# Optimization experiments

Measured on AMD Instinct MI355X. Metric: run time of the kernel, lower is better.

## Reference

```python
import jax, jax.numpy as jnp
import numpy as np

MODES = 256


def setup_inputs() -> dict:
    key = jax.random.key(0)
    k1, k2, k3, k4, k5 = jax.random.split(key, 5)
    B, C_IN, C_OUT, N, KM = 8, 128, 128, 8192, 32
    scale = 1.0 / (C_IN * C_OUT)
    return {
        "x": jax.random.normal(k1, (B, C_IN, N), dtype=jnp.float32),
        "wbases": jax.random.normal(k2, (B, N, MODES), dtype=jnp.float32),
        "bases": jax.random.normal(k3, (B, N, MODES), dtype=jnp.float32),
        "weights": scale * jax.random.normal(k4, (C_IN, C_OUT, KM), dtype=jnp.float32),
        "D": jax.random.normal(k5, (KM, MODES), dtype=jnp.float32),
    }


def reference(x, wbases, bases, weights, D):
    # Project onto weighted bases: (b, c_in, n) x (b, n, modes) -> (b, c_in, modes)
    x_hat = jnp.einsum('bcx,bxk->bck', x, wbases[:, :, :MODES])
    # D-weighted channel mixing. Original: x_hat1[b,i,j,k] = x_hat[b,i,k]*D[j,k];
    # y[b,o,k] = sum_{i,j} x_hat1[b,i,j,k] * weights[i,o,j]
    # Equivalent fused contraction (same math, no 4D broadcast):
    y_hat = jnp.einsum('bik,jk,ioj->bok', x_hat, D, weights)
    # Reconstruct on output bases: (b, c_out, modes) x (b, n, modes) -> (b, c_out, n)
    y = jnp.einsum('bck,bxk->bcx', y_hat, bases[:, :, :MODES])
    return y
```

## Files before the change

### kernel.cpp

```cpp
#include <hip/hip_runtime.h>

#define B_    8
#define CIN   128
#define COUT  128
#define NX    8192
#define KMJ   32
#define MODES 256

typedef short bf16x8 __attribute__((ext_vector_type(8)));
typedef float f32x4  __attribute__((ext_vector_type(4)));

__device__ __forceinline__ float bf2f(unsigned short u) {
    union { unsigned int i; float f; } v; v.i = ((unsigned int)u) << 16; return v.f;
}
__device__ __forceinline__ unsigned short f2bf(float f) {
    union { float f; unsigned int i; } v; v.f = f;
    unsigned int x = v.i;
    return (unsigned short)((x + 0x7fffu + ((x >> 16) & 1u)) >> 16);
}
__device__ __forceinline__ bf16x8 cvt8(const float* __restrict__ p) {
    f32x4 a = *(const f32x4*)p;
    f32x4 b = *(const f32x4*)(p + 4);
    bf16x8 r;
    r[0] = (short)f2bf(a[0]); r[1] = (short)f2bf(a[1]);
    r[2] = (short)f2bf(a[2]); r[3] = (short)f2bf(a[3]);
    r[4] = (short)f2bf(b[0]); r[5] = (short)f2bf(b[1]);
    r[6] = (short)f2bf(b[2]); r[7] = (short)f2bf(b[3]);
    return r;
}
__device__ __forceinline__ ushort4 cvt4(f32x4 a) {
    ushort4 r;
    r.x = f2bf(a[0]); r.y = f2bf(a[1]); r.z = f2bf(a[2]); r.w = f2bf(a[3]);
    return r;
}

__global__ __launch_bounds__(256) void k1_wk(const float* __restrict__ W,
                                             const float* __restrict__ D,
                                             unsigned short* __restrict__ Wk) {
    int wave = threadIdx.x >> 6, lane = threadIdx.x & 63;
    int quad = lane >> 4, l16 = lane & 15;
    int gw  = blockIdx.x * 4 + wave;
    int oi0 = gw * 16;
    int i0  = oi0 & 127, o0 = oi0 >> 7;
    bf16x8 bfrag = cvt8(W + ((size_t)(i0 + l16) * COUT + o0) * KMJ + quad * 8);
    for (int mt = 0; mt < 16; mt++) {
        int k0 = mt * 16;
        bf16x8 afrag;
#pragma unroll
        for (int jj = 0; jj < 8; jj++)
            afrag[jj] = (short)f2bf(D[(quad * 8 + jj) * MODES + k0 + l16]);
        f32x4 acc = {0.f, 0.f, 0.f, 0.f};
        acc = __builtin_amdgcn_mfma_f32_16x16x32_bf16(afrag, bfrag, acc, 0, 0, 0);
#pragma unroll
        for (int r = 0; r < 4; r++)
            Wk[(size_t)(k0 + quad * 4 + r) * (CIN * COUT) + oi0 + l16] = f2bf(acc[r]);
    }
}

__global__ __launch_bounds__(512, 4) void k2_xhat(const float* __restrict__ X,
                                                  const float* __restrict__ WB,
                                                  unsigned short* __restrict__ PART) {
    __shared__ __align__(16) unsigned short Xs[128 * 72];
    __shared__ __align__(16) unsigned short WBT[128 * 72];
    int nt = blockIdx.x, b = blockIdx.y, kh = blockIdx.z;
    int r0 = nt * 256;
    int t  = threadIdx.x;
    int wave = t >> 6, lane = t & 63;
    int wm = wave >> 2, wk = wave & 3;
    int quad = lane >> 4, l16 = lane & 15;

    const float* xb  = X  + (size_t)b * CIN * NX;
    const float* wbb = WB + (size_t)b * NX * MODES + kh * 128;

    bool isX = (t >= 256);
    int j  = t & 255;
    int xc = j & 127, xh = j >> 7;
    int kq = j & 31,  ng = j >> 5;

    f32x4 acc[4][2];
#pragma unroll
    for (int i = 0; i < 4; i++)
#pragma unroll
        for (int jj = 0; jj < 2; jj++) acc[i][jj] = (f32x4){0.f, 0.f, 0.f, 0.f};

    f32x4 st[8];

    {
        int rs = r0;
        if (isX) {
#pragma unroll
            for (int q = 0; q < 8; q++)
                st[q] = *(const f32x4*)(xb + (size_t)xc * NX + rs + xh * 32 + 4 * q);
        } else {
#pragma unroll
            for (int g = 0; g < 2; g++)
#pragma unroll
                for (int r = 0; r < 4; r++)
                    st[g * 4 + r] = *(const f32x4*)(wbb + (size_t)(rs + g * 32 + ng * 4 + r) * MODES + 4 * kq);
        }
    }

    for (int p = 0; p < 4; p++) {
        if (p) __syncthreads();
        if (isX) {
#pragma unroll
            for (int q = 0; q < 8; q++)
                *(ushort4*)(Xs + (size_t)xc * 72 + xh * 32 + 4 * q) = cvt4(st[q]);
        } else {
#pragma unroll
            for (int g = 0; g < 2; g++)
#pragma unroll
                for (int j2 = 0; j2 < 4; j2++) {
                    ushort4 w;
                    w.x = f2bf(st[g * 4 + 0][j2]); w.y = f2bf(st[g * 4 + 1][j2]);
                    w.z = f2bf(st[g * 4 + 2][j2]); w.w = f2bf(st[g * 4 + 3][j2]);
                    *(ushort4*)(WBT + (size_t)(4 * kq + j2) * 72 + g * 32 + ng * 4) = w;
                }
        }
        __syncthreads();

        if (p < 3) {
            int rs = r0 + (p + 1) * 64;
            if (isX) {
#pragma unroll
                for (int q = 0; q < 8; q++)
                    st[q] = *(const f32x4*)(xb + (size_t)xc * NX + rs + xh * 32 + 4 * q);
            } else {
#pragma unroll
                for (int g = 0; g < 2; g++)
#pragma unroll
                    for (int r = 0; r < 4; r++)
                        st[g * 4 + r] = *(const f32x4*)(wbb + (size_t)(rs + g * 32 + ng * 4 + r) * MODES + 4 * kq);
            }
        }

#pragma unroll
        for (int ks = 0; ks < 2; ks++) {
            bf16x8 af[4], bfv[2];
#pragma unroll
            for (int tm = 0; tm < 4; tm++)
                af[tm] = *(const bf16x8*)(Xs + (size_t)(wm * 64 + tm * 16 + l16) * 72 + ks * 32 + quad * 8);
#pragma unroll
            for (int tn = 0; tn < 2; tn++)
                bfv[tn] = *(const bf16x8*)(WBT + (size_t)(wk * 32 + tn * 16 + l16) * 72 + ks * 32 + quad * 8);
#pragma unroll
            for (int tm = 0; tm < 4; tm++)
#pragma unroll
                for (int tn = 0; tn < 2; tn++)
                    acc[tm][tn] = __builtin_amdgcn_mfma_f32_16x16x32_bf16(af[tm], bfv[tn], acc[tm][tn], 0, 0, 0);
        }
    }

    unsigned short* pb = PART + ((size_t)b * 32 + nt) * (CIN * MODES) + kh * 128;
#pragma unroll
    for (int tm = 0; tm < 4; tm++) {
        int c = wm * 64 + tm * 16 + quad * 4;
#pragma unroll
        for (int tn = 0; tn < 2; tn++) {
            int km = wk * 32 + tn * 16 + l16;
#pragma unroll
            for (int r = 0; r < 4; r++)
                pb[(size_t)(c + r) * MODES + km] = f2bf(acc[tm][tn][r]);
        }
    }
}

__global__ __launch_bounds__(256) void k2b_red(const unsigned short* __restrict__ PART,
                                               float* __restrict__ XH) {
    int e0 = blockIdx.x * 1024 + threadIdx.x;
#pragma unroll
    for (int r = 0; r < 4; r++) {
        int e = e0 + r * 256;
        int b = e >> 15, rem = e & 32767;
        const unsigned short* p = PART + (size_t)b * 32 * (CIN * MODES) + rem;
        float acc = 0.f;
#pragma unroll
        for (int nt = 0; nt < 32; nt++) acc += bf2f(p[nt * (CIN * MODES)]);
        XH[e] = acc;
    }
}

__global__ __launch_bounds__(256) void k3_yhat(const float* __restrict__ XH,
                                               const unsigned short* __restrict__ Wk,
                                               unsigned short* __restrict__ YH) {
    __shared__ float xs[128][8];
    int k = blockIdx.x;
    int t = threadIdx.x;
#pragma unroll
    for (int l = 0; l < 4; l++) {
        int e = l * 256 + t;
        int i = e >> 3, b = e & 7;
        xs[i][b] = XH[(size_t)b * (CIN * MODES) + (size_t)i * MODES + k];
    }
    __syncthreads();
    int o = t & 127, bh = t >> 7;
    const unsigned short* wp = Wk + (size_t)k * (CIN * COUT) + (size_t)o * CIN;
    f32x4 acc = {0.f, 0.f, 0.f, 0.f};
    for (int ii = 0; ii < 16; ii++) {
        bf16x8 wc = *(const bf16x8*)(wp + ii * 8);
#pragma unroll
        for (int jj = 0; jj < 8; jj++) {
            float w = bf2f((unsigned short)wc[jj]);
            f32x4 xv = *(const f32x4*)&xs[ii * 8 + jj][bh * 4];
            acc += w * xv;
        }
    }
#pragma unroll
    for (int r = 0; r < 4; r++)
        YH[((size_t)(bh * 4 + r) * COUT + o) * MODES + k] = f2bf(acc[r]);
}

__global__ __launch_bounds__(512, 4) void k4_y(const unsigned short* __restrict__ YH,
                                               const float* __restrict__ BA,
                                               float* __restrict__ Y) {
    __shared__ __align__(16) unsigned short As[128 * 136];
    __shared__ __align__(16) unsigned short Bs[128 * 136];
    int b  = blockIdx.y;
    int n0 = blockIdx.x * 128;
    int t  = threadIdx.x;
    int wave = t >> 6, lane = t & 63;
    int wm = wave >> 2, wn2 = wave & 3;
    int quad = lane >> 4, l16 = lane & 15;

    const unsigned short* yhb = YH + (size_t)b * COUT * MODES;
    const float* bab = BA + (size_t)b * NX * MODES + (size_t)n0 * MODES;

    int rc = t & 127, rq = t >> 7;

    f32x4 acc[4][2];
#pragma unroll
    for (int i = 0; i < 4; i++)
#pragma unroll
        for (int jj = 0; jj < 2; jj++) acc[i][jj] = (f32x4){0.f, 0.f, 0.f, 0.f};

    bf16x8 av[4];
    f32x4  bv[8];

#pragma unroll
    for (int q = 0; q < 4; q++)
        av[q] = *(const bf16x8*)(yhb + (size_t)rc * MODES + rq * 32 + 8 * q);
#pragma unroll
    for (int q = 0; q < 8; q++)
        bv[q] = *(const f32x4*)(bab + (size_t)rc * MODES + rq * 32 + 4 * q);

    for (int p = 0; p < 2; p++) {
        if (p) __syncthreads();
#pragma unroll
        for (int q = 0; q < 4; q++)
            *(bf16x8*)(As + (size_t)rc * 136 + rq * 32 + 8 * q) = av[q];
#pragma unroll
        for (int q = 0; q < 8; q++)
            *(ushort4*)(Bs + (size_t)rc * 136 + rq * 32 + 4 * q) = cvt4(bv[q]);
        __syncthreads();

        if (p == 0) {
#pragma unroll
            for (int q = 0; q < 4; q++)
                av[q] = *(const bf16x8*)(yhb + (size_t)rc * MODES + 128 + rq * 32 + 8 * q);
#pragma unroll
            for (int q = 0; q < 8; q++)
                bv[q] = *(const f32x4*)(bab + (size_t)rc * MODES + 128 + rq * 32 + 4 * q);
        }

#pragma unroll
        for (int ks = 0; ks < 4; ks++) {
            bf16x8 af[4], bfv[2];
#pragma unroll
            for (int tm = 0; tm < 4; tm++)
                af[tm] = *(const bf16x8*)(As + (size_t)(wm * 64 + tm * 16 + l16) * 136 + ks * 32 + quad * 8);
#pragma unroll
            for (int tn = 0; tn < 2; tn++)
                bfv[tn] = *(const bf16x8*)(Bs + (size_t)(wn2 * 32 + tn * 16 + l16) * 136 + ks * 32 + quad * 8);
#pragma unroll
            for (int tm = 0; tm < 4; tm++)
#pragma unroll
                for (int tn = 0; tn < 2; tn++)
                    acc[tm][tn] = __builtin_amdgcn_mfma_f32_16x16x32_bf16(af[tm], bfv[tn], acc[tm][tn], 0, 0, 0);
        }
    }

    float* yb = Y + (size_t)b * COUT * NX;
#pragma unroll
    for (int tm = 0; tm < 4; tm++) {
        int o = wm * 64 + tm * 16 + quad * 4;
#pragma unroll
        for (int tn = 0; tn < 2; tn++) {
            int n = n0 + wn2 * 32 + tn * 16 + l16;
#pragma unroll
            for (int r = 0; r < 4; r++)
                yb[(size_t)(o + r) * NX + n] = acc[tm][tn][r];
        }
    }
}

extern "C" void kernel_launch(void* const* d_in, const int* in_sizes, int n_in,
                              void* d_out, int out_size, void* d_ws, size_t ws_size,
                              hipStream_t stream) {
    const float* X  = (const float*)d_in[0];
    const float* WB = (const float*)d_in[1];
    const float* BA = (const float*)d_in[2];
    const float* W  = (const float*)d_in[3];
    const float* D  = (const float*)d_in[4];
    float* Y = (float*)d_out;

    char* ws = (char*)d_ws;
    unsigned short* Wk   = (unsigned short*)ws;
    float*          XH   = (float*)(ws + (8u << 20));
    unsigned short* YH   = (unsigned short*)(ws + (9u << 20));
    unsigned short* PART = (unsigned short*)(ws + (10u << 20));

    k1_wk  <<<256,            256, 0, stream>>>(W, D, Wk);
    k2_xhat<<<dim3(32, 8, 2), 512, 0, stream>>>(X, WB, PART);
    k2b_red<<<256,            256, 0, stream>>>(PART, XH);
    k3_yhat<<<MODES,          256, 0, stream>>>(XH, Wk, YH);
    k4_y   <<<dim3(64, 8),    512, 0, stream>>>(YH, BA, Y);
}
```

Baseline: 224.7 us.

## Raise parallelism across all kernels with smaller tiles, more threads, swizzled LDS

Every kernel gets a wider grid or larger blocks. k1 splits the mode loop across blockIdx.y. k2 and k4 move to 1024-thread blocks with 2x2 MFMA tiles per wave, 32-wide K steps with an XOR-swizzled LDS layout, and a single-register prefetch. k2b_red uses one element per thread, and k3 splits output channels over two blocks with the weights preloaded into registers. The goal is better latency hiding and occupancy in these memory-bound GEMMs, paid for with more sync rounds (8 per block instead of 4 or 2) and less register-level reuse per wave.

After: 219.5 us. -2.3%, faster.

```diff
diff --git a/kernel.cpp b/kernel.cpp
--- a/kernel.cpp
+++ b/kernel.cpp
@@ -43,8 +43,9 @@
     int oi0 = gw * 16;
     int i0  = oi0 & 127, o0 = oi0 >> 7;
     bf16x8 bfrag = cvt8(W + ((size_t)(i0 + l16) * COUT + o0) * KMJ + quad * 8);
-    for (int mt = 0; mt < 16; mt++) {
-        int k0 = mt * 16;
+#pragma unroll
+    for (int m = 0; m < 4; m++) {
+        int k0 = (blockIdx.y * 4 + m) * 16;
         bf16x8 afrag;
 #pragma unroll
         for (int jj = 0; jj < 8; jj++)
@@ -57,104 +58,80 @@
     }
 }
 
-__global__ __launch_bounds__(512, 4) void k2_xhat(const float* __restrict__ X,
-                                                  const float* __restrict__ WB,
-                                                  unsigned short* __restrict__ PART) {
-    __shared__ __align__(16) unsigned short Xs[128 * 72];
-    __shared__ __align__(16) unsigned short WBT[128 * 72];
+__global__ __launch_bounds__(1024, 8) void k2_xhat(const float* __restrict__ X,
+                                                   const float* __restrict__ WB,
+                                                   unsigned short* __restrict__ PART) {
+    __shared__ __align__(16) unsigned short Xs[128 * 40];
+    __shared__ __align__(16) unsigned short WBT[128 * 40];
     int nt = blockIdx.x, b = blockIdx.y, kh = blockIdx.z;
     int r0 = nt * 256;
     int t  = threadIdx.x;
     int wave = t >> 6, lane = t & 63;
     int wm = wave >> 2, wk = wave & 3;
     int quad = lane >> 4, l16 = lane & 15;
+    int sw = quad ^ (l16 & 3);
 
     const float* xb  = X  + (size_t)b * CIN * NX;
     const float* wbb = WB + (size_t)b * NX * MODES + kh * 128;
 
-    bool isX = (t >= 256);
-    int j  = t & 255;
-    int xc = j & 127, xh = j >> 7;
-    int kq = j & 31,  ng = j >> 5;
-
-    f32x4 acc[4][2];
-#pragma unroll
-    for (int i = 0; i < 4; i++)
+    bool isX = (t >= 512);
+    int j  = t & 511;
+    int xr = j >> 2, xseg = j & 3;
+    int kq = j >> 4, np = j & 15;
+
+    const float* gx = xb + (size_t)xr * NX + r0 + xseg * 8;
+    const float* gw = wbb + (size_t)(r0 + 2 * np) * MODES + 4 * kq;
+    unsigned short* xw = Xs + xr * 40 + ((xseg ^ (xr & 3)) << 3);
+
+    f32x4 acc[2][2];
+#pragma unroll
+    for (int i = 0; i < 2; i++)
 #pragma unroll
         for (int jj = 0; jj < 2; jj++) acc[i][jj] = (f32x4){0.f, 0.f, 0.f, 0.f};
 
-    f32x4 st[8];
-
-    {
-        int rs = r0;
-        if (isX) {
-#pragma unroll
-            for (int q = 0; q < 8; q++)
-                st[q] = *(const f32x4*)(xb + (size_t)xc * NX + rs + xh * 32 + 4 * q);
-        } else {
-#pragma unroll
-            for (int g = 0; g < 2; g++)
-#pragma unroll
-                for (int r = 0; r < 4; r++)
-                    st[g * 4 + r] = *(const f32x4*)(wbb + (size_t)(rs + g * 32 + ng * 4 + r) * MODES + 4 * kq);
-        }
-    }
-
-    for (int p = 0; p < 4; p++) {
+    f32x4 st0, st1;
+    if (isX) { st0 = *(const f32x4*)gx; st1 = *(const f32x4*)(gx + 4); }
+    else     { st0 = *(const f32x4*)gw; st1 = *(const f32x4*)(gw + MODES); }
+
+    for (int p = 0; p < 8; p++) {
         if (p) __syncthreads();
         if (isX) {
-#pragma unroll
-            for (int q = 0; q < 8; q++)
-                *(ushort4*)(Xs + (size_t)xc * 72 + xh * 32 + 4 * q) = cvt4(st[q]);
+            *(ushort4*)xw       = cvt4(st0);
+            *(ushort4*)(xw + 4) = cvt4(st1);
         } else {
 #pragma unroll
-            for (int g = 0; g < 2; g++)
-#pragma unroll
-                for (int j2 = 0; j2 < 4; j2++) {
-                    ushort4 w;
-                    w.x = f2bf(st[g * 4 + 0][j2]); w.y = f2bf(st[g * 4 + 1][j2]);
-                    w.z = f2bf(st[g * 4 + 2][j2]); w.w = f2bf(st[g * 4 + 3][j2]);
-                    *(ushort4*)(WBT + (size_t)(4 * kq + j2) * 72 + g * 32 + ng * 4) = w;
-                }
+            for (int jj = 0; jj < 4; jj++) {
+                int k = 4 * kq + jj;
+                unsigned int w = (unsigned int)f2bf(st0[jj]) |
+                                 ((unsigned int)f2bf(st1[jj]) << 16);
+                *(unsigned int*)(WBT + k * 40 + (((np >> 2) ^ (k & 3)) << 3) + ((np & 3) << 1)) = w;
+            }
         }
         __syncthreads();
 
-        if (p < 3) {
-            int rs = r0 + (p + 1) * 64;
-            if (isX) {
-#pragma unroll
-                for (int q = 0; q < 8; q++)
-                    st[q] = *(const f32x4*)(xb + (size_t)xc * NX + rs + xh * 32 + 4 * q);
-            } else {
-#pragma unroll
-                for (int g = 0; g < 2; g++)
-#pragma unroll
-                    for (int r = 0; r < 4; r++)
-                        st[g * 4 + r] = *(const f32x4*)(wbb + (size_t)(rs + g * 32 + ng * 4 + r) * MODES + 4 * kq);
-            }
-        }
-
-#pragma unroll
-        for (int ks = 0; ks < 2; ks++) {
-            bf16x8 af[4], bfv[2];
-#pragma unroll
-            for (int tm = 0; tm < 4; tm++)
-                af[tm] = *(const bf16x8*)(Xs + (size_t)(wm * 64 + tm * 16 + l16) * 72 + ks * 32 + quad * 8);
+        if (p < 7) {
+            if (isX) { gx += 32;          st0 = *(const f32x4*)gx; st1 = *(const f32x4*)(gx + 4); }
+            else     { gw += 32 * MODES;  st0 = *(const f32x4*)gw; st1 = *(const f32x4*)(gw + MODES); }
+        }
+
+        bf16x8 af[2], bfv[2];
+#pragma unroll
+        for (int tm = 0; tm < 2; tm++)
+            af[tm] = *(const bf16x8*)(Xs + (wm * 32 + tm * 16 + l16) * 40 + (sw << 3));
+#pragma unroll
+        for (int tn = 0; tn < 2; tn++)
+            bfv[tn] = *(const bf16x8*)(WBT + (wk * 32 + tn * 16 + l16) * 40 + (sw << 3));
+#pragma unroll
+        for (int tm = 0; tm < 2; tm++)
 #pragma unroll
             for (int tn = 0; tn < 2; tn++)
-                bfv[tn] = *(const bf16x8*)(WBT + (size_t)(wk * 32 + tn * 16 + l16) * 72 + ks * 32 + quad * 8);
-#pragma unroll
-            for (int tm = 0; tm < 4; tm++)
-#pragma unroll
-                for (int tn = 0; tn < 2; tn++)
-                    acc[tm][tn] = __builtin_amdgcn_mfma_f32_16x16x32_bf16(af[tm], bfv[tn], acc[tm][tn], 0, 0, 0);
-        }
+                acc[tm][tn] = __builtin_amdgcn_mfma_f32_16x16x32_bf16(af[tm], bfv[tn], acc[tm][tn], 0, 0, 0);
     }
 
     unsigned short* pb = PART + ((size_t)b * 32 + nt) * (CIN * MODES) + kh * 128;
 #pragma unroll
-    for (int tm = 0; tm < 4; tm++) {
-        int c = wm * 64 + tm * 16 + quad * 4;
+    for (int tm = 0; tm < 2; tm++) {
+        int c = wm * 32 + tm * 16 + quad * 4;
 #pragma unroll
         for (int tn = 0; tn < 2; tn++) {
             int km = wk * 32 + tn * 16 + l16;
@@ -167,125 +144,121 @@
 
 __global__ __launch_bounds__(256) void k2b_red(const unsigned short* __restrict__ PART,
                                                float* __restrict__ XH) {
-    int e0 = blockIdx.x * 1024 + threadIdx.x;
-#pragma unroll
-    for (int r = 0; r < 4; r++) {
-        int e = e0 + r * 256;
-        int b = e >> 15, rem = e & 32767;
-        const unsigned short* p = PART + (size_t)b * 32 * (CIN * MODES) + rem;
-        float acc = 0.f;
-#pragma unroll
-        for (int nt = 0; nt < 32; nt++) acc += bf2f(p[nt * (CIN * MODES)]);
-        XH[e] = acc;
-    }
-}
-
-__global__ __launch_bounds__(256) void k3_yhat(const float* __restrict__ XH,
-                                               const unsigned short* __restrict__ Wk,
-                                               unsigned short* __restrict__ YH) {
+    int e = blockIdx.x * 256 + threadIdx.x;
+    const unsigned short* p = PART + (size_t)(e >> 15) * 32 * (CIN * MODES) + (e & 32767);
+    float acc = 0.f;
+#pragma unroll
+    for (int nt = 0; nt < 32; nt++) acc += bf2f(p[nt * (CIN * MODES)]);
+    XH[e] = acc;
+}
+
+__global__ __launch_bounds__(256, 2) void k3_yhat(const float* __restrict__ XH,
+                                                  const unsigned short* __restrict__ Wk,
+                                                  unsigned short* __restrict__ YH) {
     __shared__ float xs[128][8];
-    int k = blockIdx.x;
+    int k = blockIdx.x, oh = blockIdx.y;
     int t = threadIdx.x;
 #pragma unroll
     for (int l = 0; l < 4; l++) {
         int e = l * 256 + t;
-        int i = e >> 3, b = e & 7;
-        xs[i][b] = XH[(size_t)b * (CIN * MODES) + (size_t)i * MODES + k];
-    }
+        int i = e >> 3, bb = e & 7;
+        xs[i][bb] = XH[(size_t)bb * (CIN * MODES) + (size_t)i * MODES + k];
+    }
+    int o = oh * 64 + (t & 63), bq = t >> 6;
+    const unsigned short* wp = Wk + (size_t)k * (CIN * COUT) + (size_t)o * CIN;
+    bf16x8 wc[16];
+#pragma unroll
+    for (int ii = 0; ii < 16; ii++)
+        wc[ii] = *(const bf16x8*)(wp + ii * 8);
     __syncthreads();
-    int o = t & 127, bh = t >> 7;
-    const unsigned short* wp = Wk + (size_t)k * (CIN * COUT) + (size_t)o * CIN;
-    f32x4 acc = {0.f, 0.f, 0.f, 0.f};
-    for (int ii = 0; ii < 16; ii++) {
-        bf16x8 wc = *(const bf16x8*)(wp + ii * 8);
+    float a0 = 0.f, a1 = 0.f;
+#pragma unroll
+    for (int ii = 0; ii < 16; ii++)
 #pragma unroll
         for (int jj = 0; jj < 8; jj++) {
-            float w = bf2f((unsigned short)wc[jj]);
-            f32x4 xv = *(const f32x4*)&xs[ii * 8 + jj][bh * 4];
-            acc += w * xv;
-        }
-    }
-#pragma unroll
-    for (int r = 0; r < 4; r++)
-        YH[((size_t)(bh * 4 + r) * COUT + o) * MODES + k] = f2bf(acc[r]);
-}
-
-__global__ __launch_bounds__(512, 4) void k4_y(const unsigned short* __restrict__ YH,
-                                               const float* __restrict__ BA,
-                                               float* __restrict__ Y) {
-    __shared__ __align__(16) unsigned short As[128 * 136];
-    __shared__ __align__(16) unsigned short Bs[128 * 136];
+            float w = bf2f((unsigned short)wc[ii][jj]);
+            int i = ii * 8 + jj;
+            a0 += w * xs[i][bq * 2];
+            a1 += w * xs[i][bq * 2 + 1];
+        }
+    YH[((size_t)(bq * 2)     * COUT + o) * MODES + k] = f2bf(a0);
+    YH[((size_t)(bq * 2 + 1) * COUT + o) * MODES + k] = f2bf(a1);
+}
+
+__global__ __launch_bounds__(1024, 8) void k4_y(const unsigned short* __restrict__ YH,
+                                                const float* __restrict__ BA,
+                                                float* __restrict__ Y) {
+    __shared__ __align__(16) unsigned short As[128 * 40];
+    __shared__ __align__(16) unsigned short Bs[128 * 40];
     int b  = blockIdx.y;
     int n0 = blockIdx.x * 128;
     int t  = threadIdx.x;
     int wave = t >> 6, lane = t & 63;
-    int wm = wave >> 2, wn2 = wave & 3;
+    int wm = wave >> 2, wn = wave & 3;
     int quad = lane >> 4, l16 = lane & 15;
+    int sw = quad ^ (l16 & 3);
 
     const unsigned short* yhb = YH + (size_t)b * COUT * MODES;
     const float* bab = BA + (size_t)b * NX * MODES + (size_t)n0 * MODES;
 
-    int rc = t & 127, rq = t >> 7;
-
-    f32x4 acc[4][2];
-#pragma unroll
-    for (int i = 0; i < 4; i++)
+    bool isA = (t < 512);
+    int j  = t & 511;
+    int rr = j >> 2, seg = j & 3;
+    int ssw = (seg ^ (rr & 3)) << 3;
+
+    const unsigned short* ga = yhb + (size_t)rr * MODES + seg * 8;
+    const float* gb = bab + (size_t)rr * MODES + seg * 8;
+
+    f32x4 acc[2][2];
+#pragma unroll
+    for (int i = 0; i < 2; i++)
 #pragma unroll
         for (int jj = 0; jj < 2; jj++) acc[i][jj] = (f32x4){0.f, 0.f, 0.f, 0.f};
 
-    bf16x8 av[4];
-    f32x4  bv[8];
-
-#pragma unroll
-    for (int q = 0; q < 4; q++)
-        av[q] = *(const bf16x8*)(yhb + (size_t)rc * MODES + rq * 32 + 8 * q);
-#pragma unroll
-    for (int q = 0; q < 8; q++)
-        bv[q] = *(const f32x4*)(bab + (size_t)rc * MODES + rq * 32 + 4 * q);
-
-    for (int p = 0; p < 2; p++) {
+    bf16x8 sa; f32x4 sb0, sb1;
+    if (isA) sa = *(const bf16x8*)ga;
+    else { sb0 = *(const f32x4*)gb; sb1 = *(const f32x4*)(gb + 4); }
+
+    for (int p = 0; p < 8; p++) {
         if (p) __syncthreads();
-#pragma unroll
-        for (int q = 0; q < 4; q++)
-            *(bf16x8*)(As + (size_t)rc * 136 + rq * 32 + 8 * q) = av[q];
-#pragma unroll
-        for (int q = 0; q < 8; q++)
-            *(ushort4*)(Bs + (size_t)rc * 136 + rq * 32 + 4 * q) = cvt4(bv[q]);
+        if (isA) {
+            *(bf16x8*)(As + rr * 40 + ssw) = sa;
+        } else {
+            bf16x8 v;
+            v[0] = (short)f2bf(sb0[0]); v[1] = (short)f2bf(sb0[1]);
+            v[2] = (short)f2bf(sb0[2]); v[3] = (short)f2bf(sb0[3]);
+            v[4] = (short)f2bf(sb1[0]); v[5] = (short)f2bf(sb1[1]);
+            v[6] = (short)f2bf(sb1[2]); v[7] = (short)f2bf(sb1[3]);
+            *(bf16x8*)(Bs + rr * 40 + ssw) = v;
+        }
         __syncthreads();
 
-        if (p == 0) {
-#pragma unroll
-            for (int q = 0; q < 4; q++)
-                av[q] = *(const bf16x8*)(yhb + (size_t)rc * MODES + 128 + rq * 32 + 8 * q);
-#pragma unroll
-            for (int q = 0; q < 8; q++)
-                bv[q] = *(const f32x4*)(bab + (size_t)rc * MODES + 128 + rq * 32 + 4 * q);
-        }
-
-#pragma unroll
-        for (int ks = 0; ks < 4; ks++) {
-            bf16x8 af[4], bfv[2];
-#pragma unroll
-            for (int tm = 0; tm < 4; tm++)
-                af[tm] = *(const bf16x8*)(As + (size_t)(wm * 64 + tm * 16 + l16) * 136 + ks * 32 + quad * 8);
+        if (p < 7) {
+            if (isA) { ga += 32; sa = *(const bf16x8*)ga; }
+            else     { gb += 32; sb0 = *(const f32x4*)gb; sb1 = *(const f32x4*)(gb + 4); }
+        }
+
+        bf16x8 af[2], bfv[2];
+#pragma unroll
+        for (int tm = 0; tm < 2; tm++)
+            af[tm] = *(const bf16x8*)(As + (wm * 32 + tm * 16 + l16) * 40 + (sw << 3));
+#pragma unroll
+        for (int tn = 0; tn < 2; tn++)
+            bfv[tn] = *(const bf16x8*)(Bs + (wn * 32 + tn * 16 + l16) * 40 + (sw << 3));
+#pragma unroll
+        for (int tm = 0; tm < 2; tm++)
 #pragma unroll
             for (int tn = 0; tn < 2; tn++)
-                bfv[tn] = *(const bf16x8*)(Bs + (size_t)(wn2 * 32 + tn * 16 + l16) * 136 + ks * 32 + quad * 8);
-#pragma unroll
-            for (int tm = 0; tm < 4; tm++)
-#pragma unroll
-                for (int tn = 0; tn < 2; tn++)
-                    acc[tm][tn] = __builtin_amdgcn_mfma_f32_16x16x32_bf16(af[tm], bfv[tn], acc[tm][tn], 0, 0, 0);
-        }
+                acc[tm][tn] = __builtin_amdgcn_mfma_f32_16x16x32_bf16(af[tm], bfv[tn], acc[tm][tn], 0, 0, 0);
     }
 
     float* yb = Y + (size_t)b * COUT * NX;
 #pragma unroll
-    for (int tm = 0; tm < 4; tm++) {
-        int o = wm * 64 + tm * 16 + quad * 4;
+    for (int tm = 0; tm < 2; tm++) {
+        int o = wm * 32 + tm * 16 + quad * 4;
 #pragma unroll
         for (int tn = 0; tn < 2; tn++) {
-            int n = n0 + wn2 * 32 + tn * 16 + l16;
+            int n = n0 + wn * 32 + tn * 16 + l16;
 #pragma unroll
             for (int r = 0; r < 4; r++)
                 yb[(size_t)(o + r) * NX + n] = acc[tm][tn][r];
@@ -309,9 +282,9 @@
     unsigned short* YH   = (unsigned short*)(ws + (9u << 20));
     unsigned short* PART = (unsigned short*)(ws + (10u << 20));
 
-    k1_wk  <<<256,            256, 0, stream>>>(W, D, Wk);
-    k2_xhat<<<dim3(32, 8, 2), 512, 0, stream>>>(X, WB, PART);
-    k2b_red<<<256,            256, 0, stream>>>(PART, XH);
-    k3_yhat<<<MODES,          256, 0, stream>>>(XH, Wk, YH);
-    k4_y   <<<dim3(64, 8),    512, 0, stream>>>(YH, BA, Y);
-}
+    k1_wk  <<<dim3(256, 4),   256,  0, stream>>>(W, D, Wk);
+    k2_xhat<<<dim3(32, 8, 2), 1024, 0, stream>>>(X, WB, PART);
+    k2b_red<<<1024,           256,  0, stream>>>(PART, XH);
+    k3_yhat<<<dim3(256, 2),   256,  0, stream>>>(XH, Wk, YH);
+    k4_y   <<<dim3(64, 8),    1024, 0, stream>>>(YH, BA, Y);
+}
```
